# Kernel optimization log

Measured on AMD Instinct MI355X. Metric: run time of the kernel, lower is better.

Reference implementation:

```python
import jax, jax.numpy as jnp
import numpy as np

N = 100000
E = 1600000
F_IN = 16
EPS = 1e-5


def _feast(x, src, dst, W, u, c, b, heads):
    # FeaStConv (PyG): q_h = softmax_h(u_h^T (x_j - x_i) + c_h);
    # out_i = mean_{j in N(i)} sum_h q_h * (W_h x_j) + b
    n = x.shape[0]
    out_dim = W.shape[1] // heads
    xw = (x @ W).reshape(n, heads, out_dim)              # [N,H,O]
    q = jax.nn.softmax((x[src] - x[dst]) @ u + c, axis=1)  # [E2,H]
    msg = jnp.einsum('eh,eho->eo', q, xw[src])           # [E2,O]
    agg = jax.ops.segment_sum(msg, dst, num_segments=n)
    deg = jax.ops.segment_sum(jnp.ones(dst.shape, x.dtype), dst, num_segments=n)
    return agg / jnp.maximum(deg, 1.0)[:, None] + b


def _bn(x, g, b):
    mu = x.mean(0)
    var = x.var(0)
    return (x - mu) * jax.lax.rsqrt(var + EPS) * g + b


def _forward(edge_index, x, W1, u1, c1, b1, W2, u2, c2, b2, W3, u3, c3, b3,
             W4, u4, c4, b4, W5, u5, c5, b5, W6, u6, c6, b6,
             g1, be1, g2, be2, lw1, lb1, lw2, lb2, lw3, lb3, ow, ob):
    n = x.shape[0]
    loops = jnp.arange(n)  # add_self_loops=True in FeaStConv
    src = jnp.concatenate([edge_index[0], loops])
    dst = jnp.concatenate([edge_index[1], loops])
    h = jax.nn.relu(_feast(x, src, dst, W1, u1, c1, b1, 4))
    h = _feast(h, src, dst, W2, u2, c2, b2, 4)
    h2 = h
    h = jax.nn.relu(h)
    h = jax.nn.relu(_bn(_feast(h, src, dst, W3, u3, c3, b3, 4), g1, be1))
    h = jax.nn.relu(_feast(h, src, dst, W4, u4, c4, b4, 1))
    h4 = h
    h = jax.nn.relu(_feast(h, src, dst, W5, u5, c5, b5, 1))
    h = jax.nn.relu(_bn(_feast(h, src, dst, W6, u6, c6, b6, 1), g2, be2))
    h = h + h2 + h4
    h = jax.nn.relu(h @ lw1 + lb1)
    h = jax.nn.relu(h @ lw2 + lb2)
    h = jax.nn.relu(h @ lw3 + lb3)
    return jax.nn.sigmoid(h @ ow + ob)


def setup_inputs() -> dict:
    key = jax.random.key(0)
    ks = iter(jax.random.split(key, 64))

    def rn(*s):
        return jax.random.normal(next(ks), s, jnp.float32) * 0.1

    d = {
        'x': jax.random.normal(next(ks), (N, F_IN), jnp.float32),
        'edge_index': jax.random.randint(next(ks), (2, E), 0, N),
    }
    conv_dims = [(16, 16, 4), (16, 16, 4), (16, 16, 4), (16, 16, 1), (16, 16, 1), (16, 16, 1)]
    for i, (ci, co, h) in enumerate(conv_dims, 1):
        d[f'W{i}'] = rn(ci, h * co)
        d[f'u{i}'] = rn(ci, h)
        d[f'c{i}'] = rn(h)
        d[f'b{i}'] = rn(co)
    d['g1'] = jnp.ones(16, jnp.float32); d['be1'] = jnp.zeros(16, jnp.float32)
    d['g2'] = jnp.ones(16, jnp.float32); d['be2'] = jnp.zeros(16, jnp.float32)
    d['lw1'] = rn(16, 64); d['lb1'] = rn(64)
    d['lw2'] = rn(64, 64); d['lb2'] = rn(64)
    d['lw3'] = rn(64, 16); d['lb3'] = rn(16)
    d['ow'] = rn(16, 1); d['ob'] = rn(1)
    return d


def reference(x, edge_index, W1, u1, c1, b1, W2, u2, c2, b2, W3, u3, c3, b3,
              W4, u4, c4, b4, W5, u5, c5, b5, W6, u6, c6, b6,
              g1, be1, g2, be2, lw1, lb1, lw2, lb2, lw3, lb3, ow, ob):
    return _forward(edge_index, x, W1, u1, c1, b1, W2, u2, c2, b2, W3, u3, c3, b3,
                    W4, u4, c4, b4, W5, u5, c5, b5, W6, u6, c6, b6,
                    g1, be1, g2, be2, lw1, lb1, lw2, lb2, lw3, lb3, ow, ob)
```

## Files before the change

kernel.cpp:

```cpp
#include <hip/hip_runtime.h>
#include <cmath>

#define BLK 256
#define BSHIFT 9
#define EPT 16
#define TILE (BLK * EPT)


__global__ void bhist_kernel(const int* __restrict__ dst, int* __restrict__ bcnt,
                             int E, int nbuk) {
  __shared__ int hist[256];
  int t = threadIdx.x;
  hist[t] = 0;
  __syncthreads();
  int base = blockIdx.x * TILE;
#pragma unroll
  for (int k = 0; k < EPT; k++) {
    int e = base + k * BLK + t;
    if (e < E) atomicAdd(&hist[dst[e] >> BSHIFT], 1);
  }
  __syncthreads();
  if (t < nbuk && hist[t] > 0) atomicAdd(&bcnt[t], hist[t]);
}

__global__ void bscan_kernel(const int* __restrict__ bcnt, int* __restrict__ gbase,
                             int* __restrict__ gbcur, int nbuk, int E) {
  __shared__ int sdata[BLK];
  int t = threadIdx.x;
  int v = (t < nbuk) ? bcnt[t] : 0;
  sdata[t] = v;
  __syncthreads();
  for (int off = 1; off < BLK; off <<= 1) {
    int x = (t >= off) ? sdata[t - off] : 0;
    __syncthreads();
    sdata[t] += x;
    __syncthreads();
  }
  int excl = sdata[t] - v;
  if (t < nbuk) { gbase[t] = excl; gbcur[t] = excl; }
  if (t == 0) gbase[nbuk] = E;
}

__global__ void scatter_pairs_lds_kernel(const int* __restrict__ src, const int* __restrict__ dst,
                                         int* __restrict__ gbcur, int2* __restrict__ pairs,
                                         int E, int nbuk) {
  __shared__ int hist[256];
  __shared__ int chunk[256];
  int t = threadIdx.x;
  hist[t] = 0;
  __syncthreads();
  int base = blockIdx.x * TILE;
  int es[EPT], ed[EPT];
#pragma unroll
  for (int k = 0; k < EPT; k++) {
    int e = base + k * BLK + t;
    if (e < E) {
      es[k] = src[e];
      ed[k] = dst[e];
      atomicAdd(&hist[ed[k] >> BSHIFT], 1);
    } else {
      ed[k] = -1;
    }
  }
  __syncthreads();
  if (t < nbuk && hist[t] > 0) chunk[t] = atomicAdd(&gbcur[t], hist[t]);
  __syncthreads();
#pragma unroll
  for (int k = 0; k < EPT; k++) {
    if (ed[k] >= 0) {
      int p = atomicAdd(&chunk[ed[k] >> BSHIFT], 1);
      pairs[p] = make_int2(es[k], ed[k]);
    }
  }
}

__global__ void bucket_build_kernel(const int2* __restrict__ pairs, const int* __restrict__ gbase,
                                    int* __restrict__ row_start, int* __restrict__ csr,
                                    int n, int nbuk, int E) {
  __shared__ int cnt[512];
  __shared__ int excl[512];
  __shared__ int s2[BLK];
  int b = blockIdx.x;
  int t = threadIdx.x;
  int n0 = b << BSHIFT;
  int n1 = min(n0 + (1 << BSHIFT), n);
  int bb0 = gbase[b], bb1 = gbase[b + 1];
  cnt[t] = 0; cnt[t + 256] = 0;
  __syncthreads();
  for (int r = bb0 + t; r < bb1; r += BLK) atomicAdd(&cnt[pairs[r].y - n0], 1);
  __syncthreads();
  s2[t] = cnt[2 * t] + cnt[2 * t + 1];
  __syncthreads();
  int v = s2[t];
  for (int off = 1; off < BLK; off <<= 1) {
    int x = (t >= off) ? s2[t - off] : 0;
    __syncthreads();
    s2[t] += x;
    __syncthreads();
  }
  int e2 = s2[t] - v;
  excl[2 * t] = e2;
  excl[2 * t + 1] = e2 + cnt[2 * t];
  __syncthreads();
  for (int k = t; k < n1 - n0; k += BLK) row_start[n0 + k] = bb0 + excl[k];
  if (b == nbuk - 1 && t == 0) row_start[n] = E;
  cnt[2 * t] = bb0 + excl[2 * t];
  cnt[2 * t + 1] = bb0 + excl[2 * t + 1];
  __syncthreads();
  for (int r = bb0 + t; r < bb1; r += BLK) {
    int2 pr = pairs[r];
    int pos = atomicAdd(&cnt[pr.y - n0], 1);
    csr[pos] = pr.x;
  }
}


__global__ void xu4_kernel(const float* __restrict__ x, const float* __restrict__ u,
                           float* __restrict__ xu, int n) {
  __shared__ float su[64];
  if (threadIdx.x < 64) su[threadIdx.x] = u[threadIdx.x];
  __syncthreads();
  int i = blockIdx.x * blockDim.x + threadIdx.x;
  if (i >= n) return;
  const float4* xi = (const float4*)(x + i * 16);
  float a0 = 0.f, a1 = 0.f, a2 = 0.f, a3 = 0.f;
#pragma unroll
  for (int g = 0; g < 4; g++) {
    float4 v = xi[g];
    a0 += v.x * su[(g*4+0)*4+0] + v.y * su[(g*4+1)*4+0] + v.z * su[(g*4+2)*4+0] + v.w * su[(g*4+3)*4+0];
    a1 += v.x * su[(g*4+0)*4+1] + v.y * su[(g*4+1)*4+1] + v.z * su[(g*4+2)*4+1] + v.w * su[(g*4+3)*4+1];
    a2 += v.x * su[(g*4+0)*4+2] + v.y * su[(g*4+1)*4+2] + v.z * su[(g*4+2)*4+2] + v.w * su[(g*4+3)*4+2];
    a3 += v.x * su[(g*4+0)*4+3] + v.y * su[(g*4+1)*4+3] + v.z * su[(g*4+2)*4+3] + v.w * su[(g*4+3)*4+3];
  }
  *(float4*)(xu + i * 4) = make_float4(a0, a1, a2, a3);
}

template <int EPI>
__global__ void gather4_kernel(const float* __restrict__ x, const float* __restrict__ xu,
                               const int* __restrict__ row_start, const int* __restrict__ csr,
                               const float* __restrict__ W, const float* __restrict__ c,
                               const float* __restrict__ b,
                               float* __restrict__ out, float* __restrict__ out2, int n) {
  __shared__ float4 sW[256];
  __shared__ float sc[4];
  __shared__ float sb[16];
  {
    int t = threadIdx.x;
    for (int q = t; q < 1024; q += blockDim.x) {
      int cc = q & 3, k = (q >> 2) & 15, og = (q >> 6) & 3, h = q >> 8;
      ((float*)sW)[q] = W[k * 64 + h * 16 + og * 4 + cc];
    }
    if (t < 4) sc[t] = c[t];
    if (t < 16) sb[t] = b[t];
  }
  __syncthreads();
  int tid = blockIdx.x * blockDim.x + threadIdx.x;
  int i = tid >> 3;
  int e2 = (tid >> 2) & 1;
  int f4 = tid & 3;
  if (i >= n) return;

  float4 xui = *(const float4*)(xu + i * 4);
  float acc[4][4];
#pragma unroll
  for (int h = 0; h < 4; h++)
#pragma unroll
    for (int kl = 0; kl < 4; kl++) acc[h][kl] = 0.f;

  if (e2 == 1) {
    float m = fmaxf(fmaxf(sc[0], sc[1]), fmaxf(sc[2], sc[3]));
    float q0 = __expf(sc[0] - m), q1 = __expf(sc[1] - m), q2 = __expf(sc[2] - m), q3 = __expf(sc[3] - m);
    float inv = 1.0f / (q0 + q1 + q2 + q3);
    q0 *= inv; q1 *= inv; q2 *= inv; q3 *= inv;
    float4 v = *(const float4*)(x + i * 16 + f4 * 4);
    acc[0][0] += q0 * v.x; acc[0][1] += q0 * v.y; acc[0][2] += q0 * v.z; acc[0][3] += q0 * v.w;
    acc[1][0] += q1 * v.x; acc[1][1] += q1 * v.y; acc[1][2] += q1 * v.z; acc[1][3] += q1 * v.w;
    acc[2][0] += q2 * v.x; acc[2][1] += q2 * v.y; acc[2][2] += q2 * v.z; acc[2][3] += q2 * v.w;
    acc[3][0] += q3 * v.x; acc[3][1] += q3 * v.y; acc[3][2] += q3 * v.z; acc[3][3] += q3 * v.w;
  }

  int r0 = row_start[i], r1 = row_start[i + 1];
  for (int r = r0 + e2; r < r1; r += 2) {
    int j = csr[r];
    float4 xuj = *(const float4*)(xu + j * 4);
    float l0 = xuj.x - xui.x + sc[0];
    float l1 = xuj.y - xui.y + sc[1];
    float l2 = xuj.z - xui.z + sc[2];
    float l3 = xuj.w - xui.w + sc[3];
    float m = fmaxf(fmaxf(l0, l1), fmaxf(l2, l3));
    float q0 = __expf(l0 - m), q1 = __expf(l1 - m), q2 = __expf(l2 - m), q3 = __expf(l3 - m);
    float inv = 1.0f / (q0 + q1 + q2 + q3);
    q0 *= inv; q1 *= inv; q2 *= inv; q3 *= inv;
    float4 v = *(const float4*)(x + j * 16 + f4 * 4);
    acc[0][0] += q0 * v.x; acc[0][1] += q0 * v.y; acc[0][2] += q0 * v.z; acc[0][3] += q0 * v.w;
    acc[1][0] += q1 * v.x; acc[1][1] += q1 * v.y; acc[1][2] += q1 * v.z; acc[1][3] += q1 * v.w;
    acc[2][0] += q2 * v.x; acc[2][1] += q2 * v.y; acc[2][2] += q2 * v.z; acc[2][3] += q2 * v.w;
    acc[3][0] += q3 * v.x; acc[3][1] += q3 * v.y; acc[3][2] += q3 * v.z; acc[3][3] += q3 * v.w;
  }

#pragma unroll
  for (int h = 0; h < 4; h++)
#pragma unroll
    for (int kl = 0; kl < 4; kl++) acc[h][kl] += __shfl_xor(acc[h][kl], 4);

  float p[4][4];
#pragma unroll
  for (int og = 0; og < 4; og++)
#pragma unroll
    for (int cc = 0; cc < 4; cc++) p[og][cc] = 0.f;
#pragma unroll
  for (int kl = 0; kl < 4; kl++) {
#pragma unroll
    for (int h = 0; h < 4; h++) {
      float a = acc[h][kl];
#pragma unroll
      for (int og = 0; og < 4; og++) {
        float4 w = sW[(h * 4 + og) * 16 + f4 * 4 + kl];
        p[og][0] += a * w.x; p[og][1] += a * w.y; p[og][2] += a * w.z; p[og][3] += a * w.w;
      }
    }
  }
#pragma unroll
  for (int og = 0; og < 4; og++)
#pragma unroll
    for (int cc = 0; cc < 4; cc++) {
      float v = p[og][cc];
      v += __shfl_xor(v, 1);
      v += __shfl_xor(v, 2);
      p[og][cc] = v;
    }

  if (e2 == 0) {
    float invdeg = 1.0f / (float)(r1 - r0 + 1);
    float o0, o1, o2, o3;
    if (f4 == 0)      { o0 = p[0][0]; o1 = p[0][1]; o2 = p[0][2]; o3 = p[0][3]; }
    else if (f4 == 1) { o0 = p[1][0]; o1 = p[1][1]; o2 = p[1][2]; o3 = p[1][3]; }
    else if (f4 == 2) { o0 = p[2][0]; o1 = p[2][1]; o2 = p[2][2]; o3 = p[2][3]; }
    else              { o0 = p[3][0]; o1 = p[3][1]; o2 = p[3][2]; o3 = p[3][3]; }
    o0 = o0 * invdeg + sb[f4 * 4 + 0];
    o1 = o1 * invdeg + sb[f4 * 4 + 1];
    o2 = o2 * invdeg + sb[f4 * 4 + 2];
    o3 = o3 * invdeg + sb[f4 * 4 + 3];
    if (EPI == 1) {
      *(float4*)(out + i * 16 + f4 * 4) = make_float4(o0, o1, o2, o3);
    } else if (EPI == 0) {
      *(float4*)(out + i * 16 + f4 * 4) =
          make_float4(fmaxf(o0, 0.f), fmaxf(o1, 0.f), fmaxf(o2, 0.f), fmaxf(o3, 0.f));
    } else {
      *(float4*)(out2 + i * 16 + f4 * 4) = make_float4(o0, o1, o2, o3);
      *(float4*)(out + i * 16 + f4 * 4) =
          make_float4(fmaxf(o0, 0.f), fmaxf(o1, 0.f), fmaxf(o2, 0.f), fmaxf(o3, 0.f));
    }
  }
}


template <int RELU>
__global__ void gather1_kernel(const float* __restrict__ x, const int* __restrict__ row_start,
                               const int* __restrict__ csr, const float* __restrict__ W,
                               const float* __restrict__ b, float* __restrict__ out, int n) {
  __shared__ float4 sW[64];
  __shared__ float sb[16];
  {
    int t = threadIdx.x;
    if (t < 256) {
      int cc = t & 3, k = (t >> 2) & 15, og = t >> 6;
      ((float*)sW)[t] = W[k * 16 + og * 4 + cc];
    }
    if (t < 16) sb[t] = b[t];
  }
  __syncthreads();
  int tid = blockIdx.x * blockDim.x + threadIdx.x;
  int i = tid >> 3;
  int e2 = (tid >> 2) & 1;
  int f4 = tid & 3;
  if (i >= n) return;

  float acc[4] = {0.f, 0.f, 0.f, 0.f};

  if (e2 == 1) {
    float4 v = *(const float4*)(x + i * 16 + f4 * 4);
    acc[0] += v.x; acc[1] += v.y; acc[2] += v.z; acc[3] += v.w;
  }

  int r0 = row_start[i], r1 = row_start[i + 1];
  for (int r = r0 + e2; r < r1; r += 2) {
    int j = csr[r];
    float4 v = *(const float4*)(x + j * 16 + f4 * 4);
    acc[0] += v.x; acc[1] += v.y; acc[2] += v.z; acc[3] += v.w;
  }

#pragma unroll
  for (int kl = 0; kl < 4; kl++) acc[kl] += __shfl_xor(acc[kl], 4);

  float p[4][4];
#pragma unroll
  for (int og = 0; og < 4; og++)
#pragma unroll
    for (int cc = 0; cc < 4; cc++) p[og][cc] = 0.f;
#pragma unroll
  for (int kl = 0; kl < 4; kl++) {
    float a = acc[kl];
#pragma unroll
    for (int og = 0; og < 4; og++) {
      float4 w = sW[og * 16 + f4 * 4 + kl];
      p[og][0] += a * w.x; p[og][1] += a * w.y; p[og][2] += a * w.z; p[og][3] += a * w.w;
    }
  }
#pragma unroll
  for (int og = 0; og < 4; og++)
#pragma unroll
    for (int cc = 0; cc < 4; cc++) {
      float v = p[og][cc];
      v += __shfl_xor(v, 1);
      v += __shfl_xor(v, 2);
      p[og][cc] = v;
    }

  if (e2 == 0) {
    float invdeg = 1.0f / (float)(r1 - r0 + 1);
    float o0, o1, o2, o3;
    if (f4 == 0)      { o0 = p[0][0]; o1 = p[0][1]; o2 = p[0][2]; o3 = p[0][3]; }
    else if (f4 == 1) { o0 = p[1][0]; o1 = p[1][1]; o2 = p[1][2]; o3 = p[1][3]; }
    else if (f4 == 2) { o0 = p[2][0]; o1 = p[2][1]; o2 = p[2][2]; o3 = p[2][3]; }
    else              { o0 = p[3][0]; o1 = p[3][1]; o2 = p[3][2]; o3 = p[3][3]; }
    o0 = o0 * invdeg + sb[f4 * 4 + 0];
    o1 = o1 * invdeg + sb[f4 * 4 + 1];
    o2 = o2 * invdeg + sb[f4 * 4 + 2];
    o3 = o3 * invdeg + sb[f4 * 4 + 3];
    if (RELU) {
      o0 = fmaxf(o0, 0.f); o1 = fmaxf(o1, 0.f); o2 = fmaxf(o2, 0.f); o3 = fmaxf(o3, 0.f);
    }
    *(float4*)(out + i * 16 + f4 * 4) = make_float4(o0, o1, o2, o3);
  }
}


__global__ void bn_stats_kernel(const float* __restrict__ x, float* __restrict__ stats, int n) {
  __shared__ float wbuf[4][32];
  int t = threadIdx.x;
  float ls[16], lq[16];
#pragma unroll
  for (int k = 0; k < 16; k++) { ls[k] = 0.f; lq[k] = 0.f; }
  for (int i = blockIdx.x * blockDim.x + t; i < n; i += gridDim.x * blockDim.x) {
    const float4* xi = (const float4*)(x + i * 16);
#pragma unroll
    for (int g = 0; g < 4; g++) {
      float4 v = xi[g];
      ls[g * 4 + 0] += v.x; lq[g * 4 + 0] += v.x * v.x;
      ls[g * 4 + 1] += v.y; lq[g * 4 + 1] += v.y * v.y;
      ls[g * 4 + 2] += v.z; lq[g * 4 + 2] += v.z * v.z;
      ls[g * 4 + 3] += v.w; lq[g * 4 + 3] += v.w * v.w;
    }
  }
#pragma unroll
  for (int k = 0; k < 16; k++) {
    for (int off = 1; off < 64; off <<= 1) {
      ls[k] += __shfl_xor(ls[k], off);
      lq[k] += __shfl_xor(lq[k], off);
    }
  }
  int wid = t >> 6, lane = t & 63;
  if (lane < 16) wbuf[wid][lane] = ls[lane];
  if (lane >= 16 && lane < 32) wbuf[wid][lane] = lq[lane - 16];
  __syncthreads();
  if (t < 32) {
    float s = wbuf[0][t] + wbuf[1][t] + wbuf[2][t] + wbuf[3][t];
    atomicAdd(&stats[t], s);
  }
}

template <int RESID>
__global__ void bn_apply_kernel(const float* __restrict__ x, const float* __restrict__ stats,
                                const float* __restrict__ g, const float* __restrict__ be,
                                const float* __restrict__ r1, const float* __restrict__ r2,
                                float* __restrict__ out, int n) {
  __shared__ float sscale[16], sshift[16];
  int t = threadIdx.x;
  if (t < 16) {
    float invn = 1.0f / (float)n;
    float mu = stats[t] * invn;
    float var = stats[16 + t] * invn - mu * mu;
    float sc = g[t] * rsqrtf(var + 1e-5f);
    sscale[t] = sc;
    sshift[t] = be[t] - mu * sc;
  }
  __syncthreads();
  int i = blockIdx.x * blockDim.x + t;
  if (i >= n) return;
#pragma unroll
  for (int og = 0; og < 4; og++) {
    float4 v = *(const float4*)(x + i * 16 + og * 4);
    float o0 = fmaxf(v.x * sscale[og * 4 + 0] + sshift[og * 4 + 0], 0.f);
    float o1 = fmaxf(v.y * sscale[og * 4 + 1] + sshift[og * 4 + 1], 0.f);
    float o2 = fmaxf(v.z * sscale[og * 4 + 2] + sshift[og * 4 + 2], 0.f);
    float o3 = fmaxf(v.w * sscale[og * 4 + 3] + sshift[og * 4 + 3], 0.f);
    if (RESID) {
      float4 a = *(const float4*)(r1 + i * 16 + og * 4);
      float4 bb = *(const float4*)(r2 + i * 16 + og * 4);
      o0 += a.x + bb.x; o1 += a.y + bb.y; o2 += a.z + bb.z; o3 += a.w + bb.w;
    }
    *(float4*)(out + i * 16 + og * 4) = make_float4(o0, o1, o2, o3);
  }
}


__global__ void mlp_kernel(const float* __restrict__ h,
                           const float* __restrict__ lw1, const float* __restrict__ lb1,
                           const float* __restrict__ lw2, const float* __restrict__ lb2,
                           const float* __restrict__ lw3, const float* __restrict__ lb3,
                           const float* __restrict__ ow, const float* __restrict__ ob,
                           float* __restrict__ out, int n) {
  __shared__ float4 s1[256];
  __shared__ float4 s2[1024];
  __shared__ float4 s3[256];
  __shared__ float sb1[64], sb2[64], sb3[16], sow[16], sob[1];
  {
    int t = threadIdx.x;
    for (int k = t; k < 1024; k += blockDim.x) ((float*)s1)[k] = lw1[k];
    for (int k = t; k < 4096; k += blockDim.x) ((float*)s2)[k] = lw2[k];
    for (int k = t; k < 1024; k += blockDim.x) ((float*)s3)[k] = lw3[k];
    if (t < 64) sb1[t] = lb1[t];
    if (t < 64) sb2[t] = lb2[t];
    if (t < 16) sb3[t] = lb3[t];
    if (t < 16) sow[t] = ow[t];
    if (t == 0) sob[0] = ob[0];
  }
  __syncthreads();
  int tid = blockIdx.x * blockDim.x + threadIdx.x;
  int i = tid >> 2;
  int sub = tid & 3;
  if (i >= n) return;

  float4 inq = *(const float4*)(h + i * 16 + sub * 4);
  float in4[4] = {inq.x, inq.y, inq.z, inq.w};

  float a[16];
#pragma unroll
  for (int g = 0; g < 4; g++) {
    int og = sub * 4 + g;
    a[g * 4 + 0] = sb1[og * 4 + 0]; a[g * 4 + 1] = sb1[og * 4 + 1];
    a[g * 4 + 2] = sb1[og * 4 + 2]; a[g * 4 + 3] = sb1[og * 4 + 3];
  }
#pragma unroll
  for (int k = 0; k < 16; k++) {
    float v = __shfl(in4[k & 3], k >> 2, 4);
#pragma unroll
    for (int g = 0; g < 4; g++) {
      float4 w = s1[k * 16 + sub * 4 + g];
      a[g * 4 + 0] += v * w.x; a[g * 4 + 1] += v * w.y;
      a[g * 4 + 2] += v * w.z; a[g * 4 + 3] += v * w.w;
    }
  }
#pragma unroll
  for (int k = 0; k < 16; k++) a[k] = fmaxf(a[k], 0.f);

  float b2[16];
#pragma unroll
  for (int g = 0; g < 4; g++) {
    int og = sub * 4 + g;
    b2[g * 4 + 0] = sb2[og * 4 + 0]; b2[g * 4 + 1] = sb2[og * 4 + 1];
    b2[g * 4 + 2] = sb2[og * 4 + 2]; b2[g * 4 + 3] = sb2[og * 4 + 3];
  }
#pragma unroll
  for (int k = 0; k < 64; k++) {
    float v = __shfl(a[k & 15], k >> 4, 4);
#pragma unroll
    for (int g = 0; g < 4; g++) {
      float4 w = s2[k * 16 + sub * 4 + g];
      b2[g * 4 + 0] += v * w.x; b2[g * 4 + 1] += v * w.y;
      b2[g * 4 + 2] += v * w.z; b2[g * 4 + 3] += v * w.w;
    }
  }
#pragma unroll
  for (int k = 0; k < 16; k++) b2[k] = fmaxf(b2[k], 0.f);

  float c0 = sb3[sub * 4 + 0], c1 = sb3[sub * 4 + 1], c2 = sb3[sub * 4 + 2], c3v = sb3[sub * 4 + 3];
#pragma unroll
  for (int k = 0; k < 64; k++) {
    float v = __shfl(b2[k & 15], k >> 4, 4);
    float4 w = s3[k * 4 + sub];
    c0 += v * w.x; c1 += v * w.y; c2 += v * w.z; c3v += v * w.w;
  }
  c0 = fmaxf(c0, 0.f); c1 = fmaxf(c1, 0.f); c2 = fmaxf(c2, 0.f); c3v = fmaxf(c3v, 0.f);

  float zp = c0 * sow[sub * 4 + 0] + c1 * sow[sub * 4 + 1] +
             c2 * sow[sub * 4 + 2] + c3v * sow[sub * 4 + 3];
  zp += __shfl_xor(zp, 1);
  zp += __shfl_xor(zp, 2);
  if (sub == 0) out[i] = 1.0f / (1.0f + __expf(-(zp + sob[0])));
}


extern "C" void kernel_launch(void* const* d_in, const int* in_sizes, int n_in,
                              void* d_out, int out_size, void* d_ws, size_t ws_size,
                              hipStream_t stream) {
  const float* x = (const float*)d_in[0];
  const int* ei = (const int*)d_in[1];
  const int N = in_sizes[0] / 16;
  const int E = in_sizes[1] / 2;
  const int* srcp = ei;
  const int* dstp = ei + E;

  const float* W1 = (const float*)d_in[2];  const float* u1 = (const float*)d_in[3];
  const float* c1 = (const float*)d_in[4];  const float* b1 = (const float*)d_in[5];
  const float* W2 = (const float*)d_in[6];  const float* u2 = (const float*)d_in[7];
  const float* c2 = (const float*)d_in[8];  const float* b2 = (const float*)d_in[9];
  const float* W3 = (const float*)d_in[10]; const float* u3 = (const float*)d_in[11];
  const float* c3 = (const float*)d_in[12]; const float* b3 = (const float*)d_in[13];
  const float* W4 = (const float*)d_in[14]; const float* b4 = (const float*)d_in[17];
  const float* W5 = (const float*)d_in[18]; const float* b5 = (const float*)d_in[21];
  const float* W6 = (const float*)d_in[22]; const float* b6 = (const float*)d_in[25];
  const float* g1 = (const float*)d_in[26]; const float* be1 = (const float*)d_in[27];
  const float* g2 = (const float*)d_in[28]; const float* be2 = (const float*)d_in[29];
  const float* lw1 = (const float*)d_in[30]; const float* lb1 = (const float*)d_in[31];
  const float* lw2 = (const float*)d_in[32]; const float* lb2 = (const float*)d_in[33];
  const float* lw3 = (const float*)d_in[34]; const float* lb3 = (const float*)d_in[35];
  const float* ow = (const float*)d_in[36]; const float* ob = (const float*)d_in[37];
  float* out = (float*)d_out;

  char* ws = (char*)d_ws;
  size_t off = 0;
  auto alloc = [&](size_t bytes) -> void* {
    void* p = ws + off;
    off = (off + bytes + 255) & ~(size_t)255;
    return p;
  };
  int* row_start = (int*)alloc((size_t)(N + 1) * 4);
  int* csr = (int*)alloc((size_t)E * 4);
  float* xu = (float*)alloc((size_t)N * 4 * 4);
  float* bufA = (float*)alloc((size_t)N * 16 * 4);
  float* bufB = (float*)alloc((size_t)N * 16 * 4);
  float* h2b = (float*)alloc((size_t)N * 16 * 4);
  float* h4b = (float*)alloc((size_t)N * 16 * 4);
  float* tmp = (float*)alloc((size_t)N * 16 * 4);
  float* stats = (float*)alloc(32 * 4);
  const int NBUK = (N + (1 << BSHIFT) - 1) >> BSHIFT;
  int* bcnt = (int*)alloc((size_t)NBUK * 4);
  int* gbase = (int*)alloc((size_t)(NBUK + 1) * 4);
  int* gbcur = (int*)alloc((size_t)NBUK * 4);
  int2* pairs = (int2*)bufA;

  const int NB = (N + BLK - 1) / BLK;
  const int NG4 = (4 * N + BLK - 1) / BLK;
  const int NG8 = (8 * N + BLK - 1) / BLK;
  const int NT = (E + TILE - 1) / TILE;

  hipMemsetAsync(bcnt, 0, (size_t)NBUK * 4, stream);
  bhist_kernel<<<NT, BLK, 0, stream>>>(dstp, bcnt, E, NBUK);
  bscan_kernel<<<1, BLK, 0, stream>>>(bcnt, gbase, gbcur, NBUK, E);
  scatter_pairs_lds_kernel<<<NT, BLK, 0, stream>>>(srcp, dstp, gbcur, pairs, E, NBUK);
  bucket_build_kernel<<<NBUK, BLK, 0, stream>>>(pairs, gbase, row_start, csr, N, NBUK, E);

  xu4_kernel<<<NB, BLK, 0, stream>>>(x, u1, xu, N);
  gather4_kernel<0><<<NG8, BLK, 0, stream>>>(x, xu, row_start, csr, W1, c1, b1, bufA, nullptr, N);

  xu4_kernel<<<NB, BLK, 0, stream>>>(bufA, u2, xu, N);
  gather4_kernel<2><<<NG8, BLK, 0, stream>>>(bufA, xu, row_start, csr, W2, c2, b2, bufB, h2b, N);

  xu4_kernel<<<NB, BLK, 0, stream>>>(bufB, u3, xu, N);
  gather4_kernel<1><<<NG8, BLK, 0, stream>>>(bufB, xu, row_start, csr, W3, c3, b3, tmp, nullptr, N);
  hipMemsetAsync(stats, 0, 32 * 4, stream);
  bn_stats_kernel<<<256, BLK, 0, stream>>>(tmp, stats, N);
  bn_apply_kernel<0><<<NB, BLK, 0, stream>>>(tmp, stats, g1, be1, nullptr, nullptr, bufA, N);

  gather1_kernel<1><<<NG8, BLK, 0, stream>>>(bufA, row_start, csr, W4, b4, h4b, N);

  gather1_kernel<1><<<NG8, BLK, 0, stream>>>(h4b, row_start, csr, W5, b5, bufB, N);

  gather1_kernel<0><<<NG8, BLK, 0, stream>>>(bufB, row_start, csr, W6, b6, tmp, N);
  hipMemsetAsync(stats, 0, 32 * 4, stream);
  bn_stats_kernel<<<256, BLK, 0, stream>>>(tmp, stats, N);
  bn_apply_kernel<1><<<NB, BLK, 0, stream>>>(tmp, stats, g2, be2, h2b, h4b, bufA, N);

  mlp_kernel<<<NG4, BLK, 0, stream>>>(bufA, lw1, lb1, lw2, lb2, lw3, lb3, ow, ob, out, N);
}
```

Measured before the change: 509.3 us.

## Split node features into two 8-wide planes and gather each in a separate pass

Stores every 16-float feature buffer as two 8-float planes (low and high halves) and runs each gather layer as two passes. Each pass gathers only one plane with 4 edge-parallel lanes and accumulates partial W products; the second pass adds the stored partial, normalises by degree and applies the epilogue. The aim is to shrink the random-gather working set per pass so the neighbour features fit better in cache, and csr loads become nontemporal. The cost is twice the kernel launches, twice the csr and xu traversal with repeated softmax work, an extra split kernel, and a read-modify-write of the output.

```diff
diff --git a/kernel.cpp b/kernel.cpp
--- a/kernel.cpp
+++ b/kernel.cpp
@@ -115,18 +115,35 @@
 }
 
 
-__global__ void xu4_kernel(const float* __restrict__ x, const float* __restrict__ u,
-                           float* __restrict__ xu, int n) {
-  __shared__ float su[64];
-  if (threadIdx.x < 64) su[threadIdx.x] = u[threadIdx.x];
-  __syncthreads();
+__global__ void split_x_kernel(const float* __restrict__ x, float* __restrict__ xlo,
+                               float* __restrict__ xhi, int n) {
   int i = blockIdx.x * blockDim.x + threadIdx.x;
   if (i >= n) return;
   const float4* xi = (const float4*)(x + i * 16);
+  float4 a0 = xi[0], a1 = xi[1], a2 = xi[2], a3 = xi[3];
+  *(float4*)(xlo + i * 8) = a0;
+  *(float4*)(xlo + i * 8 + 4) = a1;
+  *(float4*)(xhi + i * 8) = a2;
+  *(float4*)(xhi + i * 8 + 4) = a3;
+}
+
+
+__global__ void xu4_kernel(const float* __restrict__ xlo, const float* __restrict__ xhi,
+                           const float* __restrict__ u, float* __restrict__ xu, int n) {
+  __shared__ float su[64];
+  if (threadIdx.x < 64) su[threadIdx.x] = u[threadIdx.x];
+  __syncthreads();
+  int i = blockIdx.x * blockDim.x + threadIdx.x;
+  if (i >= n) return;
+  float4 vv[4];
+  vv[0] = *(const float4*)(xlo + i * 8);
+  vv[1] = *(const float4*)(xlo + i * 8 + 4);
+  vv[2] = *(const float4*)(xhi + i * 8);
+  vv[3] = *(const float4*)(xhi + i * 8 + 4);
   float a0 = 0.f, a1 = 0.f, a2 = 0.f, a3 = 0.f;
 #pragma unroll
   for (int g = 0; g < 4; g++) {
-    float4 v = xi[g];
+    float4 v = vv[g];
     a0 += v.x * su[(g*4+0)*4+0] + v.y * su[(g*4+1)*4+0] + v.z * su[(g*4+2)*4+0] + v.w * su[(g*4+3)*4+0];
     a1 += v.x * su[(g*4+0)*4+1] + v.y * su[(g*4+1)*4+1] + v.z * su[(g*4+2)*4+1] + v.w * su[(g*4+3)*4+1];
     a2 += v.x * su[(g*4+0)*4+2] + v.y * su[(g*4+1)*4+2] + v.z * su[(g*4+2)*4+2] + v.w * su[(g*4+3)*4+2];
@@ -135,20 +152,21 @@
   *(float4*)(xu + i * 4) = make_float4(a0, a1, a2, a3);
 }
 
-template <int EPI>
-__global__ void gather4_kernel(const float* __restrict__ x, const float* __restrict__ xu,
+template <int EPI, int PASS>
+__global__ void gather4_kernel(const float* __restrict__ xp, const float* __restrict__ xu,
                                const int* __restrict__ row_start, const int* __restrict__ csr,
                                const float* __restrict__ W, const float* __restrict__ c,
                                const float* __restrict__ b,
-                               float* __restrict__ out, float* __restrict__ out2, int n) {
-  __shared__ float4 sW[256];
+                               float* __restrict__ outlo, float* __restrict__ outhi,
+                               float* __restrict__ out2lo, float* __restrict__ out2hi, int n) {
+  __shared__ float4 sW[128];
   __shared__ float sc[4];
   __shared__ float sb[16];
   {
     int t = threadIdx.x;
-    for (int q = t; q < 1024; q += blockDim.x) {
-      int cc = q & 3, k = (q >> 2) & 15, og = (q >> 6) & 3, h = q >> 8;
-      ((float*)sW)[q] = W[k * 64 + h * 16 + og * 4 + cc];
+    for (int q = t; q < 512; q += blockDim.x) {
+      int cc = q & 3, kk = (q >> 2) & 7, og = (q >> 5) & 3, h = q >> 7;
+      ((float*)sW)[q] = W[(PASS * 8 + kk) * 64 + h * 16 + og * 4 + cc];
     }
     if (t < 4) sc[t] = c[t];
     if (t < 16) sb[t] = b[t];
@@ -156,8 +174,8 @@
   __syncthreads();
   int tid = blockIdx.x * blockDim.x + threadIdx.x;
   int i = tid >> 3;
-  int e2 = (tid >> 2) & 1;
-  int f4 = tid & 3;
+  int e4 = (tid >> 1) & 3;
+  int fh = tid & 1;
   if (i >= n) return;
 
   float4 xui = *(const float4*)(xu + i * 4);
@@ -167,12 +185,12 @@
 #pragma unroll
     for (int kl = 0; kl < 4; kl++) acc[h][kl] = 0.f;
 
-  if (e2 == 1) {
+  if (e4 == 3) {
     float m = fmaxf(fmaxf(sc[0], sc[1]), fmaxf(sc[2], sc[3]));
     float q0 = __expf(sc[0] - m), q1 = __expf(sc[1] - m), q2 = __expf(sc[2] - m), q3 = __expf(sc[3] - m);
     float inv = 1.0f / (q0 + q1 + q2 + q3);
     q0 *= inv; q1 *= inv; q2 *= inv; q3 *= inv;
-    float4 v = *(const float4*)(x + i * 16 + f4 * 4);
+    float4 v = *(const float4*)(xp + i * 8 + fh * 4);
     acc[0][0] += q0 * v.x; acc[0][1] += q0 * v.y; acc[0][2] += q0 * v.z; acc[0][3] += q0 * v.w;
     acc[1][0] += q1 * v.x; acc[1][1] += q1 * v.y; acc[1][2] += q1 * v.z; acc[1][3] += q1 * v.w;
     acc[2][0] += q2 * v.x; acc[2][1] += q2 * v.y; acc[2][2] += q2 * v.z; acc[2][3] += q2 * v.w;
@@ -180,8 +198,8 @@
   }
 
   int r0 = row_start[i], r1 = row_start[i + 1];
-  for (int r = r0 + e2; r < r1; r += 2) {
-    int j = csr[r];
+  for (int r = r0 + e4; r < r1; r += 4) {
+    int j = __builtin_nontemporal_load(csr + r);
     float4 xuj = *(const float4*)(xu + j * 4);
     float l0 = xuj.x - xui.x + sc[0];
     float l1 = xuj.y - xui.y + sc[1];
@@ -191,7 +209,7 @@
     float q0 = __expf(l0 - m), q1 = __expf(l1 - m), q2 = __expf(l2 - m), q3 = __expf(l3 - m);
     float inv = 1.0f / (q0 + q1 + q2 + q3);
     q0 *= inv; q1 *= inv; q2 *= inv; q3 *= inv;
-    float4 v = *(const float4*)(x + j * 16 + f4 * 4);
+    float4 v = *(const float4*)(xp + j * 8 + fh * 4);
     acc[0][0] += q0 * v.x; acc[0][1] += q0 * v.y; acc[0][2] += q0 * v.z; acc[0][3] += q0 * v.w;
     acc[1][0] += q1 * v.x; acc[1][1] += q1 * v.y; acc[1][2] += q1 * v.z; acc[1][3] += q1 * v.w;
     acc[2][0] += q2 * v.x; acc[2][1] += q2 * v.y; acc[2][2] += q2 * v.z; acc[2][3] += q2 * v.w;
@@ -201,7 +219,12 @@
 #pragma unroll
   for (int h = 0; h < 4; h++)
 #pragma unroll
-    for (int kl = 0; kl < 4; kl++) acc[h][kl] += __shfl_xor(acc[h][kl], 4);
+    for (int kl = 0; kl < 4; kl++) {
+      float v = acc[h][kl];
+      v += __shfl_xor(v, 2);
+      v += __shfl_xor(v, 4);
+      acc[h][kl] = v;
+    }
 
   float p[4][4];
 #pragma unroll
@@ -215,7 +238,7 @@
       float a = acc[h][kl];
 #pragma unroll
       for (int og = 0; og < 4; og++) {
-        float4 w = sW[(h * 4 + og) * 16 + f4 * 4 + kl];
+        float4 w = sW[(h * 4 + og) * 8 + fh * 4 + kl];
         p[og][0] += a * w.x; p[og][1] += a * w.y; p[og][2] += a * w.z; p[og][3] += a * w.w;
       }
     }
@@ -223,75 +246,85 @@
 #pragma unroll
   for (int og = 0; og < 4; og++)
 #pragma unroll
-    for (int cc = 0; cc < 4; cc++) {
-      float v = p[og][cc];
-      v += __shfl_xor(v, 1);
-      v += __shfl_xor(v, 2);
-      p[og][cc] = v;
-    }
-
-  if (e2 == 0) {
-    float invdeg = 1.0f / (float)(r1 - r0 + 1);
+    for (int cc = 0; cc < 4; cc++) p[og][cc] += __shfl_xor(p[og][cc], 1);
+
+  if (fh == 0) {
+    int og = e4;
     float o0, o1, o2, o3;
-    if (f4 == 0)      { o0 = p[0][0]; o1 = p[0][1]; o2 = p[0][2]; o3 = p[0][3]; }
-    else if (f4 == 1) { o0 = p[1][0]; o1 = p[1][1]; o2 = p[1][2]; o3 = p[1][3]; }
-    else if (f4 == 2) { o0 = p[2][0]; o1 = p[2][1]; o2 = p[2][2]; o3 = p[2][3]; }
+    if (og == 0)      { o0 = p[0][0]; o1 = p[0][1]; o2 = p[0][2]; o3 = p[0][3]; }
+    else if (og == 1) { o0 = p[1][0]; o1 = p[1][1]; o2 = p[1][2]; o3 = p[1][3]; }
+    else if (og == 2) { o0 = p[2][0]; o1 = p[2][1]; o2 = p[2][2]; o3 = p[2][3]; }
     else              { o0 = p[3][0]; o1 = p[3][1]; o2 = p[3][2]; o3 = p[3][3]; }
-    o0 = o0 * invdeg + sb[f4 * 4 + 0];
-    o1 = o1 * invdeg + sb[f4 * 4 + 1];
-    o2 = o2 * invdeg + sb[f4 * 4 + 2];
-    o3 = o3 * invdeg + sb[f4 * 4 + 3];
-    if (EPI == 1) {
-      *(float4*)(out + i * 16 + f4 * 4) = make_float4(o0, o1, o2, o3);
-    } else if (EPI == 0) {
-      *(float4*)(out + i * 16 + f4 * 4) =
-          make_float4(fmaxf(o0, 0.f), fmaxf(o1, 0.f), fmaxf(o2, 0.f), fmaxf(o3, 0.f));
+    float* plane = (og < 2) ? outlo : outhi;
+    int addr = i * 8 + (og & 1) * 4;
+    if (PASS == 0) {
+      *(float4*)(plane + addr) = make_float4(o0, o1, o2, o3);
     } else {
-      *(float4*)(out2 + i * 16 + f4 * 4) = make_float4(o0, o1, o2, o3);
-      *(float4*)(out + i * 16 + f4 * 4) =
-          make_float4(fmaxf(o0, 0.f), fmaxf(o1, 0.f), fmaxf(o2, 0.f), fmaxf(o3, 0.f));
-    }
-  }
-}
-
-
-template <int RELU>
-__global__ void gather1_kernel(const float* __restrict__ x, const int* __restrict__ row_start,
+      float4 prev = *(const float4*)(plane + addr);
+      float invdeg = 1.0f / (float)(r1 - r0 + 1);
+      o0 = (o0 + prev.x) * invdeg + sb[og * 4 + 0];
+      o1 = (o1 + prev.y) * invdeg + sb[og * 4 + 1];
+      o2 = (o2 + prev.z) * invdeg + sb[og * 4 + 2];
+      o3 = (o3 + prev.w) * invdeg + sb[og * 4 + 3];
+      if (EPI == 1) {
+        *(float4*)(plane + addr) = make_float4(o0, o1, o2, o3);
+      } else if (EPI == 0) {
+        *(float4*)(plane + addr) =
+            make_float4(fmaxf(o0, 0.f), fmaxf(o1, 0.f), fmaxf(o2, 0.f), fmaxf(o3, 0.f));
+      } else {
+        float* plane2 = (og < 2) ? out2lo : out2hi;
+        *(float4*)(plane2 + addr) = make_float4(o0, o1, o2, o3);
+        *(float4*)(plane + addr) =
+            make_float4(fmaxf(o0, 0.f), fmaxf(o1, 0.f), fmaxf(o2, 0.f), fmaxf(o3, 0.f));
+      }
+    }
+  }
+}
+
+
+template <int RELU, int PASS>
+__global__ void gather1_kernel(const float* __restrict__ xp, const int* __restrict__ row_start,
                                const int* __restrict__ csr, const float* __restrict__ W,
-                               const float* __restrict__ b, float* __restrict__ out, int n) {
-  __shared__ float4 sW[64];
+                               const float* __restrict__ b,
+                               float* __restrict__ outlo, float* __restrict__ outhi, int n) {
+  __shared__ float4 sW[32];
   __shared__ float sb[16];
   {
     int t = threadIdx.x;
-    if (t < 256) {
-      int cc = t & 3, k = (t >> 2) & 15, og = t >> 6;
-      ((float*)sW)[t] = W[k * 16 + og * 4 + cc];
+    if (t < 128) {
+      int cc = t & 3, kk = (t >> 2) & 7, og = t >> 5;
+      ((float*)sW)[t] = W[(PASS * 8 + kk) * 16 + og * 4 + cc];
     }
     if (t < 16) sb[t] = b[t];
   }
   __syncthreads();
   int tid = blockIdx.x * blockDim.x + threadIdx.x;
   int i = tid >> 3;
-  int e2 = (tid >> 2) & 1;
-  int f4 = tid & 3;
+  int e4 = (tid >> 1) & 3;
+  int fh = tid & 1;
   if (i >= n) return;
 
   float acc[4] = {0.f, 0.f, 0.f, 0.f};
 
-  if (e2 == 1) {
-    float4 v = *(const float4*)(x + i * 16 + f4 * 4);
+  if (e4 == 3) {
+    float4 v = *(const float4*)(xp + i * 8 + fh * 4);
     acc[0] += v.x; acc[1] += v.y; acc[2] += v.z; acc[3] += v.w;
   }
 
   int r0 = row_start[i], r1 = row_start[i + 1];
-  for (int r = r0 + e2; r < r1; r += 2) {
-    int j = csr[r];
-    float4 v = *(const float4*)(x + j * 16 + f4 * 4);
+  for (int r = r0 + e4; r < r1; r += 4) {
+    int j = __builtin_nontemporal_load(csr + r);
+    float4 v = *(const float4*)(xp + j * 8 + fh * 4);
     acc[0] += v.x; acc[1] += v.y; acc[2] += v.z; acc[3] += v.w;
   }
 
 #pragma unroll
-  for (int kl = 0; kl < 4; kl++) acc[kl] += __shfl_xor(acc[kl], 4);
+  for (int kl = 0; kl < 4; kl++) {
+    float v = acc[kl];
+    v += __shfl_xor(v, 2);
+    v += __shfl_xor(v, 4);
+    acc[kl] = v;
+  }
 
   float p[4][4];
 #pragma unroll
@@ -303,50 +336,58 @@
     float a = acc[kl];
 #pragma unroll
     for (int og = 0; og < 4; og++) {
-      float4 w = sW[og * 16 + f4 * 4 + kl];
+      float4 w = sW[og * 8 + fh * 4 + kl];
       p[og][0] += a * w.x; p[og][1] += a * w.y; p[og][2] += a * w.z; p[og][3] += a * w.w;
     }
   }
 #pragma unroll
   for (int og = 0; og < 4; og++)
 #pragma unroll
-    for (int cc = 0; cc < 4; cc++) {
-      float v = p[og][cc];
-      v += __shfl_xor(v, 1);
-      v += __shfl_xor(v, 2);
-      p[og][cc] = v;
-    }
-
-  if (e2 == 0) {
-    float invdeg = 1.0f / (float)(r1 - r0 + 1);
+    for (int cc = 0; cc < 4; cc++) p[og][cc] += __shfl_xor(p[og][cc], 1);
+
+  if (fh == 0) {
+    int og = e4;
     float o0, o1, o2, o3;
-    if (f4 == 0)      { o0 = p[0][0]; o1 = p[0][1]; o2 = p[0][2]; o3 = p[0][3]; }
-    else if (f4 == 1) { o0 = p[1][0]; o1 = p[1][1]; o2 = p[1][2]; o3 = p[1][3]; }
-    else if (f4 == 2) { o0 = p[2][0]; o1 = p[2][1]; o2 = p[2][2]; o3 = p[2][3]; }
+    if (og == 0)      { o0 = p[0][0]; o1 = p[0][1]; o2 = p[0][2]; o3 = p[0][3]; }
+    else if (og == 1) { o0 = p[1][0]; o1 = p[1][1]; o2 = p[1][2]; o3 = p[1][3]; }
+    else if (og == 2) { o0 = p[2][0]; o1 = p[2][1]; o2 = p[2][2]; o3 = p[2][3]; }
     else              { o0 = p[3][0]; o1 = p[3][1]; o2 = p[3][2]; o3 = p[3][3]; }
-    o0 = o0 * invdeg + sb[f4 * 4 + 0];
-    o1 = o1 * invdeg + sb[f4 * 4 + 1];
-    o2 = o2 * invdeg + sb[f4 * 4 + 2];
-    o3 = o3 * invdeg + sb[f4 * 4 + 3];
-    if (RELU) {
-      o0 = fmaxf(o0, 0.f); o1 = fmaxf(o1, 0.f); o2 = fmaxf(o2, 0.f); o3 = fmaxf(o3, 0.f);
-    }
-    *(float4*)(out + i * 16 + f4 * 4) = make_float4(o0, o1, o2, o3);
-  }
-}
-
-
-__global__ void bn_stats_kernel(const float* __restrict__ x, float* __restrict__ stats, int n) {
+    float* plane = (og < 2) ? outlo : outhi;
+    int addr = i * 8 + (og & 1) * 4;
+    if (PASS == 0) {
+      *(float4*)(plane + addr) = make_float4(o0, o1, o2, o3);
+    } else {
+      float4 prev = *(const float4*)(plane + addr);
+      float invdeg = 1.0f / (float)(r1 - r0 + 1);
+      o0 = (o0 + prev.x) * invdeg + sb[og * 4 + 0];
+      o1 = (o1 + prev.y) * invdeg + sb[og * 4 + 1];
+      o2 = (o2 + prev.z) * invdeg + sb[og * 4 + 2];
+      o3 = (o3 + prev.w) * invdeg + sb[og * 4 + 3];
+      if (RELU) {
+        o0 = fmaxf(o0, 0.f); o1 = fmaxf(o1, 0.f); o2 = fmaxf(o2, 0.f); o3 = fmaxf(o3, 0.f);
+      }
+      *(float4*)(plane + addr) = make_float4(o0, o1, o2, o3);
+    }
+  }
+}
+
+
+__global__ void bn_stats_kernel(const float* __restrict__ xlo, const float* __restrict__ xhi,
+                                float* __restrict__ stats, int n) {
   __shared__ float wbuf[4][32];
   int t = threadIdx.x;
   float ls[16], lq[16];
 #pragma unroll
   for (int k = 0; k < 16; k++) { ls[k] = 0.f; lq[k] = 0.f; }
   for (int i = blockIdx.x * blockDim.x + t; i < n; i += gridDim.x * blockDim.x) {
-    const float4* xi = (const float4*)(x + i * 16);
+    float4 vv[4];
+    vv[0] = *(const float4*)(xlo + i * 8);
+    vv[1] = *(const float4*)(xlo + i * 8 + 4);
+    vv[2] = *(const float4*)(xhi + i * 8);
+    vv[3] = *(const float4*)(xhi + i * 8 + 4);
 #pragma unroll
     for (int g = 0; g < 4; g++) {
-      float4 v = xi[g];
+      float4 v = vv[g];
       ls[g * 4 + 0] += v.x; lq[g * 4 + 0] += v.x * v.x;
       ls[g * 4 + 1] += v.y; lq[g * 4 + 1] += v.y * v.y;
       ls[g * 4 + 2] += v.z; lq[g * 4 + 2] += v.z * v.z;
@@ -371,10 +412,12 @@
 }
 
 template <int RESID>
-__global__ void bn_apply_kernel(const float* __restrict__ x, const float* __restrict__ stats,
+__global__ void bn_apply_kernel(const float* __restrict__ xlo, const float* __restrict__ xhi,
+                                const float* __restrict__ stats,
                                 const float* __restrict__ g, const float* __restrict__ be,
-                                const float* __restrict__ r1, const float* __restrict__ r2,
-                                float* __restrict__ out, int n) {
+                                const float* __restrict__ r1lo, const float* __restrict__ r1hi,
+                                const float* __restrict__ r2lo, const float* __restrict__ r2hi,
+                                float* __restrict__ outlo, float* __restrict__ outhi, int n) {
   __shared__ float sscale[16], sshift[16];
   int t = threadIdx.x;
   if (t < 16) {
@@ -390,22 +433,27 @@
   if (i >= n) return;
 #pragma unroll
   for (int og = 0; og < 4; og++) {
-    float4 v = *(const float4*)(x + i * 16 + og * 4);
+    const float* xpl = (og < 2) ? xlo : xhi;
+    float* opl = (og < 2) ? outlo : outhi;
+    int addr = i * 8 + (og & 1) * 4;
+    float4 v = *(const float4*)(xpl + addr);
     float o0 = fmaxf(v.x * sscale[og * 4 + 0] + sshift[og * 4 + 0], 0.f);
     float o1 = fmaxf(v.y * sscale[og * 4 + 1] + sshift[og * 4 + 1], 0.f);
     float o2 = fmaxf(v.z * sscale[og * 4 + 2] + sshift[og * 4 + 2], 0.f);
     float o3 = fmaxf(v.w * sscale[og * 4 + 3] + sshift[og * 4 + 3], 0.f);
     if (RESID) {
-      float4 a = *(const float4*)(r1 + i * 16 + og * 4);
-      float4 bb = *(const float4*)(r2 + i * 16 + og * 4);
+      const float* r1p = (og < 2) ? r1lo : r1hi;
+      const float* r2p = (og < 2) ? r2lo : r2hi;
+      float4 a = *(const float4*)(r1p + addr);
+      float4 bb = *(const float4*)(r2p + addr);
       o0 += a.x + bb.x; o1 += a.y + bb.y; o2 += a.z + bb.z; o3 += a.w + bb.w;
     }
-    *(float4*)(out + i * 16 + og * 4) = make_float4(o0, o1, o2, o3);
-  }
-}
-
-
-__global__ void mlp_kernel(const float* __restrict__ h,
+    *(float4*)(opl + addr) = make_float4(o0, o1, o2, o3);
+  }
+}
+
+
+__global__ void mlp_kernel(const float* __restrict__ hlo, const float* __restrict__ hhi,
                            const float* __restrict__ lw1, const float* __restrict__ lb1,
                            const float* __restrict__ lw2, const float* __restrict__ lb2,
                            const float* __restrict__ lw3, const float* __restrict__ lb3,
@@ -432,7 +480,8 @@
   int sub = tid & 3;
   if (i >= n) return;
 
-  float4 inq = *(const float4*)(h + i * 16 + sub * 4);
+  const float* base = ((sub < 2) ? hlo : hhi) + i * 8 + (sub & 1) * 4;
+  float4 inq = *(const float4*)base;
   float in4[4] = {inq.x, inq.y, inq.z, inq.w};
 
   float a[16];
@@ -526,52 +575,61 @@
     off = (off + bytes + 255) & ~(size_t)255;
     return p;
   };
+  const size_t PL = (size_t)N * 8 * 4;
   int* row_start = (int*)alloc((size_t)(N + 1) * 4);
   int* csr = (int*)alloc((size_t)E * 4);
   float* xu = (float*)alloc((size_t)N * 4 * 4);
-  float* bufA = (float*)alloc((size_t)N * 16 * 4);
-  float* bufB = (float*)alloc((size_t)N * 16 * 4);
-  float* h2b = (float*)alloc((size_t)N * 16 * 4);
-  float* h4b = (float*)alloc((size_t)N * 16 * 4);
-  float* tmp = (float*)alloc((size_t)N * 16 * 4);
+  float* A_lo = (float*)alloc(PL); float* A_hi = (float*)alloc(PL);
+  float* B_lo = (float*)alloc(PL); float* B_hi = (float*)alloc(PL);
+  float* h2_lo = (float*)alloc(PL); float* h2_hi = (float*)alloc(PL);
+  float* h4_lo = (float*)alloc(PL); float* h4_hi = (float*)alloc(PL);
+  float* T_lo = (float*)alloc(PL); float* T_hi = (float*)alloc(PL);
+  float* x_lo = (float*)alloc(PL); float* x_hi = (float*)alloc(PL);
   float* stats = (float*)alloc(32 * 4);
   const int NBUK = (N + (1 << BSHIFT) - 1) >> BSHIFT;
   int* bcnt = (int*)alloc((size_t)NBUK * 4);
   int* gbase = (int*)alloc((size_t)(NBUK + 1) * 4);
   int* gbcur = (int*)alloc((size_t)NBUK * 4);
-  int2* pairs = (int2*)bufA;
+  int2* pairs = (int2*)A_lo;
 
   const int NB = (N + BLK - 1) / BLK;
   const int NG4 = (4 * N + BLK - 1) / BLK;
   const int NG8 = (8 * N + BLK - 1) / BLK;
   const int NT = (E + TILE - 1) / TILE;
 
+  split_x_kernel<<<NB, BLK, 0, stream>>>(x, x_lo, x_hi, N);
   hipMemsetAsync(bcnt, 0, (size_t)NBUK * 4, stream);
   bhist_kernel<<<NT, BLK, 0, stream>>>(dstp, bcnt, E, NBUK);
   bscan_kernel<<<1, BLK, 0, stream>>>(bcnt, gbase, gbcur, NBUK, E);
   scatter_pairs_lds_kernel<<<NT, BLK, 0, stream>>>(srcp, dstp, gbcur, pairs, E, NBUK);
   bucket_build_kernel<<<NBUK, BLK, 0, stream>>>(pairs, gbase, row_start, csr, N, NBUK, E);
 
-  xu4_kernel<<<NB, BLK, 0, stream>>>(x, u1, xu, N);
-  gather4_kernel<0><<<NG8, BLK, 0, stream>>>(x, xu, row_start, csr, W1, c1, b1, bufA, nullptr, N);
-
-  xu4_kernel<<<NB, BLK, 0, stream>>>(bufA, u2, xu, N);
-  gather4_kernel<2><<<NG8, BLK, 0, stream>>>(bufA, xu, row_start, csr, W2, c2, b2, bufB, h2b, N);
-
-  xu4_kernel<<<NB, BLK, 0, stream>>>(bufB, u3, xu, N);
-  gather4_kernel<1><<<NG8, BLK, 0, stream>>>(bufB, xu, row_start, csr, W3, c3, b3, tmp, nullptr, N);
+  xu4_kernel<<<NB, BLK, 0, stream>>>(x_lo, x_hi, u1, xu, N);
+  gather4_kernel<0, 0><<<NG8, BLK, 0, stream>>>(x_lo, xu, row_start, csr, W1, c1, b1, A_lo, A_hi, nullptr, nullptr, N);
+  gather4_kernel<0, 1><<<NG8, BLK, 0, stream>>>(x_hi, xu, row_start, csr, W1, c1, b1, A_lo, A_hi, nullptr, nullptr, N);
+
+  xu4_kernel<<<NB, BLK, 0, stream>>>(A_lo, A_hi, u2, xu, N);
+  gather4_kernel<2, 0><<<NG8, BLK, 0, stream>>>(A_lo, xu, row_start, csr, W2, c2, b2, B_lo, B_hi, h2_lo, h2_hi, N);
+  gather4_kernel<2, 1><<<NG8, BLK, 0, stream>>>(A_hi, xu, row_start, csr, W2, c2, b2, B_lo, B_hi, h2_lo, h2_hi, N);
+
+  xu4_kernel<<<NB, BLK, 0, stream>>>(B_lo, B_hi, u3, xu, N);
+  gather4_kernel<1, 0><<<NG8, BLK, 0, stream>>>(B_lo, xu, row_start, csr, W3, c3, b3, T_lo, T_hi, nullptr, nullptr, N);
+  gather4_kernel<1, 1><<<NG8, BLK, 0, stream>>>(B_hi, xu, row_start, csr, W3, c3, b3, T_lo, T_hi, nullptr, nullptr, N);
   hipMemsetAsync(stats, 0, 32 * 4, stream);
-  bn_stats_kernel<<<256, BLK, 0, stream>>>(tmp, stats, N);
-  bn_apply_kernel<0><<<NB, BLK, 0, stream>>>(tmp, stats, g1, be1, nullptr, nullptr, bufA, N);
-
-  gather1_kernel<1><<<NG8, BLK, 0, stream>>>(bufA, row_start, csr, W4, b4, h4b, N);
-
-  gather1_kernel<1><<<NG8, BLK, 0, stream>>>(h4b, row_start, csr, W5, b5, bufB, N);
-
-  gather1_kernel<0><<<NG8, BLK, 0, stream>>>(bufB, row_start, csr, W6, b6, tmp, N);
+  bn_stats_kernel<<<256, BLK, 0, stream>>>(T_lo, T_hi, stats, N);
+  bn_apply_kernel<0><<<NB, BLK, 0, stream>>>(T_lo, T_hi, stats, g1, be1, nullptr, nullptr, nullptr, nullptr, A_lo, A_hi, N);
+
+  gather1_kernel<1, 0><<<NG8, BLK, 0, stream>>>(A_lo, row_start, csr, W4, b4, h4_lo, h4_hi, N);
+  gather1_kernel<1, 1><<<NG8, BLK, 0, stream>>>(A_hi, row_start, csr, W4, b4, h4_lo, h4_hi, N);
+
+  gather1_kernel<1, 0><<<NG8, BLK, 0, stream>>>(h4_lo, row_start, csr, W5, b5, B_lo, B_hi, N);
+  gather1_kernel<1, 1><<<NG8, BLK, 0, stream>>>(h4_hi, row_start, csr, W5, b5, B_lo, B_hi, N);
+
+  gather1_kernel<0, 0><<<NG8, BLK, 0, stream>>>(B_lo, row_start, csr, W6, b6, T_lo, T_hi, N);
+  gather1_kernel<0, 1><<<NG8, BLK, 0, stream>>>(B_hi, row_start, csr, W6, b6, T_lo, T_hi, N);
   hipMemsetAsync(stats, 0, 32 * 4, stream);
-  bn_stats_kernel<<<256, BLK, 0, stream>>>(tmp, stats, N);
-  bn_apply_kernel<1><<<NB, BLK, 0, stream>>>(tmp, stats, g2, be2, h2b, h4b, bufA, N);
-
-  mlp_kernel<<<NG4, BLK, 0, stream>>>(bufA, lw1, lb1, lw2, lb2, lw3, lb3, ow, ob, out, N);
-}
+  bn_stats_kernel<<<256, BLK, 0, stream>>>(T_lo, T_hi, stats, N);
+  bn_apply_kernel<1><<<NB, BLK, 0, stream>>>(T_lo, T_hi, stats, g2, be2, h2_lo, h2_hi, h4_lo, h4_hi, A_lo, A_hi, N);
+
+  mlp_kernel<<<NG4, BLK, 0, stream>>>(A_lo, A_hi, lw1, lb1, lw2, lb2, lw3, lb3, ow, ob, out, N);
+}
```

New measurement: 676.8 us. +32.9%, slower.
